# Performance work log

Measured on AMD Instinct MI355X. Metric: run time of the kernel, lower is better.

The kernel has to match this reference:

```python
import jax, jax.numpy as jnp
import numpy as np

B, L, D, H, W = 32, 1024, 512, 8, 5  # batch, seq, d_model, heads, local_context_length
DK = D // H


def _local_mix(x, W0, b0, w):
    """Sliding-window local-context weighting (faithful to the torch loop version).
    Pads front with w-1 zeros, applies linear (so padded rows become the bias),
    softmax-weights each length-w causal window against the current position,
    and sums the window.  x: [B, L, D] -> [B, L, D]."""
    Bb, Ll, Dd = x.shape
    xp = jnp.pad(x, ((0, 0), (w - 1, 0), (0, 0)))          # [B, L+w-1, D]
    xp = xp @ W0 + b0                                       # linear AFTER pad (padded rows = bias)
    idx = jnp.arange(Ll)[:, None] + jnp.arange(w)[None, :]  # [L, w] window indices into padded seq
    win = xp[:, idx, :]                                     # [B, L, w, D]
    cur = xp[:, w - 1:, :]                                  # [B, L, D] current positions
    scores = jnp.einsum('bld,blwd->blw', cur, win) / jnp.sqrt(jnp.float32(Dd))
    wts = jax.nn.softmax(scores, axis=-1)                   # [B, L, w]
    return jnp.einsum('blw,blwd->bld', wts, win)            # [B, L, D]


def setup_inputs() -> dict:
    rng = jax.random.key(0)
    ks = jax.random.split(rng, 7)
    s = 0.02
    return {
        'query': jax.random.normal(ks[0], (B, L, D), jnp.float32),
        'key':   jax.random.normal(ks[1], (B, L, D), jnp.float32),
        'value': jax.random.normal(ks[2], (B, L, D), jnp.float32),
        'W0':    jax.random.normal(ks[3], (D, D), jnp.float32) * s,
        'b0':    jax.random.normal(ks[4], (D,), jnp.float32) * s,
        'Wout':  jax.random.normal(ks[5], (D, D), jnp.float32) * s,
        'bout':  jax.random.normal(ks[6], (D,), jnp.float32) * s,
    }


def reference(query, key, value, W0, b0, Wout, bout):
    q = _local_mix(query, W0, b0, W).reshape(B, L, H, DK).transpose(0, 2, 1, 3)  # [B,H,L,dk]
    k = _local_mix(key, W0, b0, W).reshape(B, L, H, DK).transpose(0, 2, 1, 3)
    v = (value @ W0 + b0).reshape(B, L, H, DK).transpose(0, 2, 1, 3)
    scores = jnp.einsum('bhqd,bhkd->bhqk', q, k) / jnp.sqrt(jnp.float32(DK))     # [B,H,L,L]
    p = jax.nn.softmax(scores, axis=-1)
    x = jnp.einsum('bhqk,bhkd->bhqd', p, v)
    x = x.transpose(0, 2, 1, 3).reshape(B, L, D)
    return x @ Wout + bout
```

## Files before the change

### kernel.cpp

```cpp
#include <hip/hip_runtime.h>


typedef __attribute__((ext_vector_type(8))) short bf16x8;
typedef __attribute__((ext_vector_type(4))) float f32x4;

#define MFMA16(a, b, c) __builtin_amdgcn_mfma_f32_16x16x32_bf16((a), (b), (c), 0, 0, 0)

static __device__ __forceinline__ float bf2f(unsigned short u) {
  union { unsigned int i; float f; } v; v.i = ((unsigned int)u) << 16; return v.f;
}
static __device__ __forceinline__ unsigned short f2b(float f) {
  union { float fv; unsigned int i; } v; v.fv = f;
  unsigned int u = v.i;
  return (unsigned short)((u + 0x7fffu + ((u >> 16) & 1u)) >> 16);
}
static __device__ __forceinline__ unsigned int cvtpk(float lo, float hi) {
  unsigned int r;
  asm("v_cvt_pk_bf16_f32 %0, %1, %2" : "=v"(r) : "v"(lo), "v"(hi));
  return r;
}
static __device__ __forceinline__ void glds16(const void* g, void* l) {
  __builtin_amdgcn_global_load_lds(
      (const __attribute__((address_space(1))) unsigned int*)g,
      (__attribute__((address_space(3))) unsigned int*)l, 16, 0, 0);
}

__global__ __launch_bounds__(256) void tcast2_k(const float* __restrict__ s0,
                                                unsigned short* __restrict__ d0,
                                                const float* __restrict__ s1,
                                                unsigned short* __restrict__ d1) {
  int i = blockIdx.x * 256 + threadIdx.x;
  const float* s = s0;
  unsigned short* d = d0;
  if (i >= 262144) { i -= 262144; s = s1; d = d1; }
  int k = i >> 9, n = i & 511;
  d[(size_t)n * 512 + k] = f2b(s[(size_t)k * 512 + n]);
}

template <int AMODE, int OUTMODE>
__device__ __forceinline__ void gemm_body(const void* __restrict__ A_,
                                          const unsigned short* __restrict__ BT,
                                          const float* __restrict__ bias,
                                          void* __restrict__ out_, int bm, int bn) {
  constexpr int TSZ = (AMODE == 0) ? 16384 : 8192;
  __shared__ __align__(16) char As[2][TSZ];
  const int tid = threadIdx.x;
  const int w = tid >> 6, l = tid & 63;
  const int lg = l >> 4, lr = l & 15;
  const int wr = w >> 1, wc = w & 1;
  const int rowbase = bm * 128;
  const int colbase = bn * 128 + wc * 64;

  f32x4 acc[4][4];
#pragma unroll
  for (int m = 0; m < 4; ++m)
#pragma unroll
    for (int n = 0; n < 4; ++n) acc[m][n] = (f32x4){0.f, 0.f, 0.f, 0.f};

  auto stage = [&](int kt, int buf) {
    if constexpr (AMODE == 0) {
      const float* Af = (const float*)A_;
#pragma unroll
      for (int j = 0; j < 4; ++j) {
        const int rb = w * 32 + j * 8;
        const int r = rb + (l >> 3);
        const int gsrc = (l & 7) ^ (r & 7);
        glds16(Af + (size_t)(rowbase + r) * 512 + kt * 32 + gsrc * 4,
               &As[buf][rb * 128]);
      }
    } else {
      const unsigned short* Ab = (const unsigned short*)A_;
#pragma unroll
      for (int j = 0; j < 2; ++j) {
        const int rb = w * 32 + j * 16;
        const int r = rb + (l >> 2);
        const int gsrc = (l & 3) ^ (r & 3) ^ ((r >> 2) & 3);
        glds16(Ab + (size_t)(rowbase + r) * 512 + kt * 32 + gsrc * 8,
               &As[buf][rb * 64]);
      }
    }
  };

  stage(0, 0);
  __syncthreads();

  for (int kt = 0; kt < 16; ++kt) {
    const int cur = kt & 1;
    bf16x8 bf[4];
#pragma unroll
    for (int n = 0; n < 4; ++n)
      bf[n] = *(const bf16x8*)(BT + (size_t)(colbase + n * 16 + lr) * 512 + kt * 32 + lg * 8);
    if (kt < 15) stage(kt + 1, cur ^ 1);
    bf16x8 af[4];
#pragma unroll
    for (int m = 0; m < 4; ++m) {
      const int r = wr * 64 + m * 16 + lr;
      if constexpr (AMODE == 0) {
        const char* Ro = &As[cur][r * 128];
        const int x = r & 7;
        const float4 a0 = *(const float4*)(Ro + ((((2 * lg) ^ x)) << 4));
        const float4 a1 = *(const float4*)(Ro + ((((2 * lg + 1) ^ x)) << 4));
        union { uint4 d; bf16x8 v; } u;
        u.d.x = cvtpk(a0.x, a0.y); u.d.y = cvtpk(a0.z, a0.w);
        u.d.z = cvtpk(a1.x, a1.y); u.d.w = cvtpk(a1.z, a1.w);
        af[m] = u.v;
      } else {
        const int gsw = lg ^ (r & 3) ^ ((r >> 2) & 3);
        af[m] = *(const bf16x8*)(&As[cur][r * 64 + (gsw << 4)]);
      }
    }
    __builtin_amdgcn_s_setprio(1);
#pragma unroll
    for (int m = 0; m < 4; ++m)
#pragma unroll
      for (int n = 0; n < 4; ++n) acc[m][n] = MFMA16(af[m], bf[n], acc[m][n]);
    __builtin_amdgcn_s_setprio(0);
    __syncthreads();
  }

#pragma unroll
  for (int m = 0; m < 4; ++m)
#pragma unroll
    for (int n = 0; n < 4; ++n) {
      const int grow0 = rowbase + wr * 64 + m * 16 + 4 * lg;
      const int gcol = colbase + n * 16 + lr;
      const float bs = bias[gcol];
#pragma unroll
      for (int r = 0; r < 4; ++r) {
        float v = acc[m][n][r] + bs;
        if constexpr (OUTMODE == 0)
          ((unsigned short*)out_)[(size_t)(grow0 + r) * 512 + gcol] = f2b(v);
        else
          ((float*)out_)[(size_t)(grow0 + r) * 512 + gcol] = v;
      }
    }
}

__global__ __launch_bounds__(256) void proj3_k(const float* __restrict__ q,
                                               const float* __restrict__ k,
                                               const float* __restrict__ v,
                                               const unsigned short* __restrict__ W0T,
                                               const float* __restrict__ b0,
                                               unsigned short* __restrict__ Pq,
                                               unsigned short* __restrict__ Pk,
                                               unsigned short* __restrict__ Pv) {
  const int wg = (blockIdx.x & 7) * 384 + (blockIdx.x >> 3);
  const int t = wg >> 10, rem = wg & 1023;
  const float* A = t == 0 ? q : t == 1 ? k : v;
  unsigned short* O = t == 0 ? Pq : t == 1 ? Pk : Pv;
  gemm_body<0, 0>(A, W0T, b0, O, rem >> 2, rem & 3);
}

__global__ __launch_bounds__(256) void gemmout_k(const unsigned short* __restrict__ A,
                                                 const unsigned short* __restrict__ WoT,
                                                 const float* __restrict__ bout,
                                                 float* __restrict__ out) {
  const int wg = (blockIdx.x & 7) * 128 + (blockIdx.x >> 3);
  gemm_body<1, 1>(A, WoT, bout, out, wg >> 2, wg & 3);
}

__global__ __launch_bounds__(256) void localmix2_k(const unsigned short* __restrict__ Pq,
                                                   const unsigned short* __restrict__ Pk,
                                                   const float* __restrict__ b0,
                                                   unsigned short* __restrict__ Qm,
                                                   unsigned short* __restrict__ Km) {
  const int w = threadIdx.x >> 6, lane = threadIdx.x & 63;
  const int pp = blockIdx.x * 4 + w;
  const unsigned short* P;
  unsigned short* out;
  float outscale;
  int p;
  if (pp < 32768) { P = Pq; out = Qm; outscale = 0.18033688011112042f; p = pp; }
  else            { P = Pk; out = Km; outscale = 1.0f; p = pp - 32768; }
  const int l = p & 1023;
  const int d0 = lane * 8;

  float win[5][8];
#pragma unroll
  for (int j = 0; j < 5; ++j) {
    const int src = l - 4 + j;
    if (src >= 0) {
      const uint4 v = *(const uint4*)(P + (size_t)(p - 4 + j) * 512 + d0);
      const unsigned short* u = (const unsigned short*)&v;
#pragma unroll
      for (int i = 0; i < 8; ++i) win[j][i] = bf2f(u[i]);
    } else {
      const float4 f0 = *(const float4*)(b0 + d0);
      const float4 f1 = *(const float4*)(b0 + d0 + 4);
      win[j][0] = f0.x; win[j][1] = f0.y; win[j][2] = f0.z; win[j][3] = f0.w;
      win[j][4] = f1.x; win[j][5] = f1.y; win[j][6] = f1.z; win[j][7] = f1.w;
    }
  }
  float s[5];
#pragma unroll
  for (int j = 0; j < 5; ++j) {
    float t = 0.f;
#pragma unroll
    for (int i = 0; i < 8; ++i) t += win[4][i] * win[j][i];
    s[j] = t;
  }
#pragma unroll
  for (int off = 1; off < 64; off <<= 1)
#pragma unroll
    for (int j = 0; j < 5; ++j) s[j] += __shfl_xor(s[j], off, 64);
  const float sc = 0.04419417382415922f;
  float mx = -1e30f;
#pragma unroll
  for (int j = 0; j < 5; ++j) { s[j] *= sc; mx = fmaxf(mx, s[j]); }
  float e[5], sum = 0.f;
#pragma unroll
  for (int j = 0; j < 5; ++j) { e[j] = __expf(s[j] - mx); sum += e[j]; }
  const float inv = 1.f / sum;
  __attribute__((ext_vector_type(8))) unsigned short o;
#pragma unroll
  for (int i = 0; i < 8; ++i) {
    float a = 0.f;
#pragma unroll
    for (int j = 0; j < 5; ++j) a += e[j] * win[j][i];
    o[i] = f2b(a * inv * outscale);
  }
  *(__attribute__((ext_vector_type(8))) unsigned short*)(out + (size_t)p * 512 + d0) = o;
}

__global__ __launch_bounds__(256) void attn_k(const unsigned short* __restrict__ Q,
                                              const unsigned short* __restrict__ K,
                                              const unsigned short* __restrict__ V,
                                              unsigned short* __restrict__ AO) {
  __shared__ unsigned short Ks[2][64 * 64];
  __shared__ unsigned short Vt[2][64 * 64];
  const int tid = threadIdx.x;
  const int w = tid >> 6, l = tid & 63;
  const int lg = l >> 4, lr = l & 15;
  const int wg = (blockIdx.x & 7) * 256 + (blockIdx.x >> 3);
  const int qt = wg & 7, bh = wg >> 3;
  const int h = bh & 7, b = bh >> 3;
  const size_t base = (size_t)(b * 1024) * 512 + h * 64;
  const unsigned short* Qb = Q + base + (size_t)(qt * 128) * 512;
  const unsigned short* Kb = K + base;
  const unsigned short* Vb = V + base;

  bf16x8 qf[2][2];
#pragma unroll
  for (int rb = 0; rb < 2; ++rb)
#pragma unroll
    for (int ks = 0; ks < 2; ++ks)
      qf[rb][ks] = *(const bf16x8*)(Qb + (size_t)(w * 32 + rb * 16 + lr) * 512 + ks * 32 + lg * 8);

  f32x4 acc[2][4];
#pragma unroll
  for (int rb = 0; rb < 2; ++rb)
#pragma unroll
    for (int nb = 0; nb < 4; ++nb) acc[rb][nb] = (f32x4){0.f, 0.f, 0.f, 0.f};
  float lrun[2] = {0.f, 0.f};

  const int sk_row = tid >> 2, sk_seg = tid & 3;
  const int sv_key = tid & 63, sv_d0 = (tid >> 6) * 16;
  const int vpos = (sv_key & 32) + ((sv_key >> 2) & 3) * 8 + ((sv_key >> 4) & 1) * 4 + (sv_key & 3);
  const int vpg = vpos >> 3, vpw = vpos & 7;
  const int r7 = sk_row & 7;

  uint4 kr0, kr1, vr0, vr1;
  auto loadT = [&](int t) {
    const uint4* ksrc = (const uint4*)(Kb + (size_t)(t * 64 + sk_row) * 512 + sk_seg * 16);
    kr0 = ksrc[0]; kr1 = ksrc[1];
    const uint4* vsrc = (const uint4*)(Vb + (size_t)(t * 64 + sv_key) * 512 + sv_d0);
    vr0 = vsrc[0]; vr1 = vsrc[1];
  };
  auto writeT = [&](int bufi) {
    unsigned short* kd = Ks[bufi];
    unsigned short* vd = Vt[bufi];
    *(uint4*)&kd[sk_row * 64 + (((2 * sk_seg) ^ r7) << 3)] = kr0;
    *(uint4*)&kd[sk_row * 64 + (((2 * sk_seg + 1) ^ r7) << 3)] = kr1;
    const unsigned short* u0 = (const unsigned short*)&vr0;
    const unsigned short* u1 = (const unsigned short*)&vr1;
#pragma unroll
    for (int j = 0; j < 8; ++j) {
      vd[(sv_d0 + j) * 64 + (((vpg ^ j) << 3) | vpw)] = u0[j];
      vd[(sv_d0 + 8 + j) * 64 + (((vpg ^ j) << 3) | vpw)] = u1[j];
    }
  };

  loadT(0);
  writeT(0);
  loadT(1);
  __syncthreads();

  const int swz0 = (lg ^ (lr & 7)) << 3, swz1 = ((4 + lg) ^ (lr & 7)) << 3;

  for (int it = 0; it < 16; ++it) {
    const int cur = it & 1;
    f32x4 sf[2][4];
    __builtin_amdgcn_s_setprio(1);
#pragma unroll
    for (int kb = 0; kb < 4; ++kb) {
      const int krow = (kb * 16 + lr) * 64;
      bf16x8 kf0 = *(const bf16x8*)&Ks[cur][krow + swz0];
      bf16x8 kf1 = *(const bf16x8*)&Ks[cur][krow + swz1];
#pragma unroll
      for (int rb = 0; rb < 2; ++rb) {
        f32x4 z = (f32x4){0.f, 0.f, 0.f, 0.f};
        z = MFMA16(kf0, qf[rb][0], z);
        z = MFMA16(kf1, qf[rb][1], z);
        sf[rb][kb] = z;
      }
    }
    __builtin_amdgcn_s_setprio(0);

    if (it < 15) writeT((it + 1) & 1);
    if (it < 14) loadT(it + 2);

#pragma unroll
    for (int rb = 0; rb < 2; ++rb) {
#pragma unroll
      for (int kb = 0; kb < 4; ++kb)
#pragma unroll
        for (int r = 0; r < 4; ++r)
          sf[rb][kb][r] = __builtin_amdgcn_exp2f(sf[rb][kb][r]);
      float s0 = (sf[rb][0][0] + sf[rb][0][1]) + (sf[rb][0][2] + sf[rb][0][3]);
      float s1 = (sf[rb][1][0] + sf[rb][1][1]) + (sf[rb][1][2] + sf[rb][1][3]);
      float s2 = (sf[rb][2][0] + sf[rb][2][1]) + (sf[rb][2][2] + sf[rb][2][3]);
      float s3 = (sf[rb][3][0] + sf[rb][3][1]) + (sf[rb][3][2] + sf[rb][3][3]);
      float t = (s0 + s1) + (s2 + s3);
      t += __shfl_xor(t, 16, 64);
      t += __shfl_xor(t, 32, 64);
      lrun[rb] += t;
    }

    union { uint4 d; bf16x8 v; } pa[2][2];
#pragma unroll
    for (int rb = 0; rb < 2; ++rb)
#pragma unroll
      for (int t2 = 0; t2 < 2; ++t2) {
        pa[rb][t2].d.x = cvtpk(sf[rb][2 * t2][0], sf[rb][2 * t2][1]);
        pa[rb][t2].d.y = cvtpk(sf[rb][2 * t2][2], sf[rb][2 * t2][3]);
        pa[rb][t2].d.z = cvtpk(sf[rb][2 * t2 + 1][0], sf[rb][2 * t2 + 1][1]);
        pa[rb][t2].d.w = cvtpk(sf[rb][2 * t2 + 1][2], sf[rb][2 * t2 + 1][3]);
      }

    __builtin_amdgcn_s_setprio(1);
#pragma unroll
    for (int t2 = 0; t2 < 2; ++t2) {
      bf16x8 vf[4];
#pragma unroll
      for (int nb = 0; nb < 4; ++nb) {
        const int vrow = (nb * 16 + lr) * 64;
        vf[nb] = *(const bf16x8*)&Vt[cur][vrow + (((4 * t2 + lg) ^ (lr & 7)) << 3)];
      }
#pragma unroll
      for (int rb = 0; rb < 2; ++rb)
#pragma unroll
        for (int nb = 0; nb < 4; ++nb) acc[rb][nb] = MFMA16(pa[rb][t2].v, vf[nb], acc[rb][nb]);
    }
    __builtin_amdgcn_s_setprio(0);
    if (it < 15) __syncthreads();
  }

#pragma unroll
  for (int rb = 0; rb < 2; ++rb) {
    const float rec = 1.f / lrun[rb];
    float lv[4];
#pragma unroll
    for (int r = 0; r < 4; ++r) lv[r] = __shfl(rec, lg * 4 + r, 64);
#pragma unroll
    for (int nb = 0; nb < 4; ++nb) {
      const int gcol = nb * 16 + lr;
#pragma unroll
      for (int r = 0; r < 4; ++r) {
        const int grow = qt * 128 + w * 32 + rb * 16 + 4 * lg + r;
        AO[base + (size_t)grow * 512 + gcol] = f2b(acc[rb][nb][r] * lv[r]);
      }
    }
  }
}

extern "C" void kernel_launch(void* const* d_in, const int* in_sizes, int n_in,
                              void* d_out, int out_size, void* d_ws, size_t ws_size,
                              hipStream_t stream) {
  const float* query = (const float*)d_in[0];
  const float* key   = (const float*)d_in[1];
  const float* value = (const float*)d_in[2];
  const float* W0    = (const float*)d_in[3];
  const float* b0    = (const float*)d_in[4];
  const float* Wout  = (const float*)d_in[5];
  const float* bout  = (const float*)d_in[6];
  float* out = (float*)d_out;

  char* ws = (char*)d_ws;
  const size_t PSZ = (size_t)32768 * 512 * 2;
  unsigned short* Pq  = (unsigned short*)(ws);
  unsigned short* Pk  = (unsigned short*)(ws + PSZ);
  unsigned short* Pv  = (unsigned short*)(ws + 2 * PSZ);
  unsigned short* Qm  = (unsigned short*)(ws + 3 * PSZ);
  unsigned short* Km  = (unsigned short*)(ws + 4 * PSZ);
  unsigned short* W0T = (unsigned short*)(ws + 5 * PSZ);
  unsigned short* WoT = (unsigned short*)(ws + 5 * PSZ + 524288);

  tcast2_k<<<2048, 256, 0, stream>>>(W0, W0T, Wout, WoT);
  proj3_k<<<3072, 256, 0, stream>>>(query, key, value, W0T, b0, Pq, Pk, Pv);
  localmix2_k<<<16384, 256, 0, stream>>>(Pq, Pk, b0, Qm, Km);
  attn_k<<<2048, 256, 0, stream>>>(Qm, Km, Pv, Pq );
  gemmout_k<<<1024, 256, 0, stream>>>(Pq, WoT, bout, out);
}
```

Baseline: 339.1 us.

## Single-buffer GEMM staging, drop XCD swizzle, use lighter barrier in attention

The projection and output GEMMs go from a double-buffered LDS prefetch to a single buffer. Each k-step now stages its tile and then synchronises, so there is no longer any overlap between the global-to-LDS load and the MFMA work. The block-index remap that spread workgroups across XCDs is removed, along with the setprio hints around the MFMA loop. In the attention kernel, __syncthreads is replaced by an explicit lgkmcnt wait plus s_barrier and sched_barrier, which may avoid waiting on outstanding global loads at each barrier.

```diff
diff --git a/kernel.cpp b/kernel.cpp
--- a/kernel.cpp
+++ b/kernel.cpp
@@ -23,6 +23,11 @@
   __builtin_amdgcn_global_load_lds(
       (const __attribute__((address_space(1))) unsigned int*)g,
       (__attribute__((address_space(3))) unsigned int*)l, 16, 0, 0);
+}
+static __device__ __forceinline__ void barrier_lgkm() {
+  asm volatile("s_waitcnt lgkmcnt(0)" ::: "memory");
+  __builtin_amdgcn_s_barrier();
+  __builtin_amdgcn_sched_barrier(0);
 }
 
 __global__ __launch_bounds__(256) void tcast2_k(const float* __restrict__ s0,
@@ -43,7 +48,7 @@
                                           const float* __restrict__ bias,
                                           void* __restrict__ out_, int bm, int bn) {
   constexpr int TSZ = (AMODE == 0) ? 16384 : 8192;
-  __shared__ __align__(16) char As[2][TSZ];
+  __shared__ __align__(16) char As[TSZ];
   const int tid = threadIdx.x;
   const int w = tid >> 6, l = tid & 63;
   const int lg = l >> 4, lr = l & 15;
@@ -57,7 +62,7 @@
 #pragma unroll
     for (int n = 0; n < 4; ++n) acc[m][n] = (f32x4){0.f, 0.f, 0.f, 0.f};
 
-  auto stage = [&](int kt, int buf) {
+  auto stage = [&](int kt) {
     if constexpr (AMODE == 0) {
       const float* Af = (const float*)A_;
 #pragma unroll
@@ -66,7 +71,7 @@
         const int r = rb + (l >> 3);
         const int gsrc = (l & 7) ^ (r & 7);
         glds16(Af + (size_t)(rowbase + r) * 512 + kt * 32 + gsrc * 4,
-               &As[buf][rb * 128]);
+               &As[rb * 128]);
       }
     } else {
       const unsigned short* Ab = (const unsigned short*)A_;
@@ -76,45 +81,40 @@
         const int r = rb + (l >> 2);
         const int gsrc = (l & 3) ^ (r & 3) ^ ((r >> 2) & 3);
         glds16(Ab + (size_t)(rowbase + r) * 512 + kt * 32 + gsrc * 8,
-               &As[buf][rb * 64]);
+               &As[rb * 64]);
       }
     }
   };
 
-  stage(0, 0);
-  __syncthreads();
-
   for (int kt = 0; kt < 16; ++kt) {
-    const int cur = kt & 1;
+    stage(kt);
     bf16x8 bf[4];
 #pragma unroll
     for (int n = 0; n < 4; ++n)
       bf[n] = *(const bf16x8*)(BT + (size_t)(colbase + n * 16 + lr) * 512 + kt * 32 + lg * 8);
-    if (kt < 15) stage(kt + 1, cur ^ 1);
+    __syncthreads();
     bf16x8 af[4];
 #pragma unroll
     for (int m = 0; m < 4; ++m) {
       const int r = wr * 64 + m * 16 + lr;
       if constexpr (AMODE == 0) {
-        const char* Ro = &As[cur][r * 128];
+        const char* Ro = &As[r * 128];
         const int x = r & 7;
-        const float4 a0 = *(const float4*)(Ro + ((((2 * lg) ^ x)) << 4));
-        const float4 a1 = *(const float4*)(Ro + ((((2 * lg + 1) ^ x)) << 4));
+        const float4 a0 = *(const float4*)(Ro + (((2 * lg) ^ x) << 4));
+        const float4 a1 = *(const float4*)(Ro + (((2 * lg + 1) ^ x) << 4));
         union { uint4 d; bf16x8 v; } u;
         u.d.x = cvtpk(a0.x, a0.y); u.d.y = cvtpk(a0.z, a0.w);
         u.d.z = cvtpk(a1.x, a1.y); u.d.w = cvtpk(a1.z, a1.w);
         af[m] = u.v;
       } else {
         const int gsw = lg ^ (r & 3) ^ ((r >> 2) & 3);
-        af[m] = *(const bf16x8*)(&As[cur][r * 64 + (gsw << 4)]);
-      }
-    }
-    __builtin_amdgcn_s_setprio(1);
+        af[m] = *(const bf16x8*)(&As[r * 64 + (gsw << 4)]);
+      }
+    }
 #pragma unroll
     for (int m = 0; m < 4; ++m)
 #pragma unroll
       for (int n = 0; n < 4; ++n) acc[m][n] = MFMA16(af[m], bf[n], acc[m][n]);
-    __builtin_amdgcn_s_setprio(0);
     __syncthreads();
   }
 
@@ -144,7 +144,7 @@
                                                unsigned short* __restrict__ Pq,
                                                unsigned short* __restrict__ Pk,
                                                unsigned short* __restrict__ Pv) {
-  const int wg = (blockIdx.x & 7) * 384 + (blockIdx.x >> 3);
+  const int wg = blockIdx.x;
   const int t = wg >> 10, rem = wg & 1023;
   const float* A = t == 0 ? q : t == 1 ? k : v;
   unsigned short* O = t == 0 ? Pq : t == 1 ? Pk : Pv;
@@ -155,7 +155,7 @@
                                                  const unsigned short* __restrict__ WoT,
                                                  const float* __restrict__ bout,
                                                  float* __restrict__ out) {
-  const int wg = (blockIdx.x & 7) * 128 + (blockIdx.x >> 3);
+  const int wg = blockIdx.x;
   gemm_body<1, 1>(A, WoT, bout, out, wg >> 2, wg & 3);
 }
 
@@ -283,7 +283,7 @@
   loadT(0);
   writeT(0);
   loadT(1);
-  __syncthreads();
+  barrier_lgkm();
 
   const int swz0 = (lg ^ (lr & 7)) << 3, swz1 = ((4 + lg) ^ (lr & 7)) << 3;
 
@@ -352,7 +352,7 @@
         for (int nb = 0; nb < 4; ++nb) acc[rb][nb] = MFMA16(pa[rb][t2].v, vf[nb], acc[rb][nb]);
     }
     __builtin_amdgcn_s_setprio(0);
-    if (it < 15) __syncthreads();
+    if (it < 15) barrier_lgkm();
   }
 
 #pragma unroll
```

Measured after the change: 349.0 us. +2.9%, slower.
